# Kernel tuning notes

Hardware: AMD Instinct MI355X
Metric: run time of the kernel (lower is better)

## Reference

```python
import jax, jax.numpy as jnp
import numpy as np

N = 8_000_000  # batch rows; feature dims (1->2->...->2->1) are fixed by P1


def setup_inputs() -> dict:
    key = jax.random.key(0)
    ks = jax.random.split(key, 7)
    return {
        "x": jax.random.normal(ks[0], (N, 1), dtype=jnp.float32),
        "w_in": jax.random.normal(ks[1], (2, 1), dtype=jnp.float32),
        "b_in": jax.random.normal(ks[2], (2,), dtype=jnp.float32),
        "w_hid": jax.random.normal(ks[3], (8, 2, 2), dtype=jnp.float32),
        "b_hid": jax.random.normal(ks[4], (8, 2), dtype=jnp.float32),
        "w_out": jax.random.normal(ks[5], (1, 2), dtype=jnp.float32),
        "b_out": jax.random.normal(ks[6], (1,), dtype=jnp.float32),
    }


def _block(h, W, b):
    # Linear_BasicBlock: y = relu(h @ W.T + b)  (torch nn.Linear convention)
    return jax.nn.relu(jnp.matmul(h, W.T) + b)


def reference(x, w_in, b_in, w_hid, b_hid, w_out, b_out):
    h = _block(x, w_in, b_in)                    # [N,1] -> [N,2]

    def step(h, wb):
        W, b = wb
        return _block(h, W, b), None             # [N,2] -> [N,2]

    h, _ = jax.lax.scan(step, h, (w_hid, b_hid)) # 8 hidden blocks
    out = _block(h, w_out, b_out)                # [N,2] -> [N,1]
    return out
```

## Files before the change

kernel.cpp:

```cpp
#include <hip/hip_runtime.h>

#define NHID 8

__global__ __launch_bounds__(256) void P1_mlp_kernel(
    const float* __restrict__ x,
    const float* __restrict__ w_in, const float* __restrict__ b_in,
    const float* __restrict__ w_hid, const float* __restrict__ b_hid,
    const float* __restrict__ w_out, const float* __restrict__ b_out,
    float* __restrict__ out, int n)
{
    const float wi0 = w_in[0], wi1 = w_in[1];
    const float bi0 = b_in[0], bi1 = b_in[1];
    float wh[NHID][4];
    float bh[NHID][2];
#pragma unroll
    for (int l = 0; l < NHID; ++l) {
        wh[l][0] = w_hid[l * 4 + 0];
        wh[l][1] = w_hid[l * 4 + 1];
        wh[l][2] = w_hid[l * 4 + 2];
        wh[l][3] = w_hid[l * 4 + 3];
        bh[l][0] = b_hid[l * 2 + 0];
        bh[l][1] = b_hid[l * 2 + 1];
    }
    const float wo0 = w_out[0], wo1 = w_out[1], bo = b_out[0];

    const int tid = blockIdx.x * blockDim.x + threadIdx.x;
    const int stride = gridDim.x * blockDim.x;
    const int nv = n >> 2;

    const float4* __restrict__ x4 = (const float4*)x;
    float4* __restrict__ o4 = (float4*)out;

    for (int i = tid; i < nv; i += stride) {
        const float4 xv = x4[i];
        float xin[4] = {xv.x, xv.y, xv.z, xv.w};
        float r[4];
#pragma unroll
        for (int e = 0; e < 4; ++e) {
            float h0 = fmaxf(fmaf(xin[e], wi0, bi0), 0.0f);
            float h1 = fmaxf(fmaf(xin[e], wi1, bi1), 0.0f);
#pragma unroll
            for (int l = 0; l < NHID; ++l) {
                float n0 = fmaxf(fmaf(h1, wh[l][1], fmaf(h0, wh[l][0], bh[l][0])), 0.0f);
                float n1 = fmaxf(fmaf(h1, wh[l][3], fmaf(h0, wh[l][2], bh[l][1])), 0.0f);
                h0 = n0;
                h1 = n1;
            }
            r[e] = fmaxf(fmaf(h1, wo1, fmaf(h0, wo0, bo)), 0.0f);
        }
        float4 ov;
        ov.x = r[0]; ov.y = r[1]; ov.z = r[2]; ov.w = r[3];
        o4[i] = ov;
    }

    const int tail_base = nv << 2;
    const int tail_n = n - tail_base;
    if (tid < tail_n) {
        const float xx = x[tail_base + tid];
        float h0 = fmaxf(fmaf(xx, wi0, bi0), 0.0f);
        float h1 = fmaxf(fmaf(xx, wi1, bi1), 0.0f);
#pragma unroll
        for (int l = 0; l < NHID; ++l) {
            float n0 = fmaxf(fmaf(h1, wh[l][1], fmaf(h0, wh[l][0], bh[l][0])), 0.0f);
            float n1 = fmaxf(fmaf(h1, wh[l][3], fmaf(h0, wh[l][2], bh[l][1])), 0.0f);
            h0 = n0;
            h1 = n1;
        }
        out[tail_base + tid] = fmaxf(fmaf(h1, wo1, fmaf(h0, wo0, bo)), 0.0f);
    }
}

extern "C" void kernel_launch(void* const* d_in, const int* in_sizes, int n_in,
                              void* d_out, int out_size, void* d_ws, size_t ws_size,
                              hipStream_t stream) {
    const float* x     = (const float*)d_in[0];
    const float* w_in  = (const float*)d_in[1];
    const float* b_in  = (const float*)d_in[2];
    const float* w_hid = (const float*)d_in[3];
    const float* b_hid = (const float*)d_in[4];
    const float* w_out = (const float*)d_in[5];
    const float* b_out = (const float*)d_in[6];
    float* out = (float*)d_out;

    const int n = in_sizes[0];
    const int nv = (n + 3) / 4;
    const int block = 256;
    int grid = (nv + block - 1) / block;
    if (grid > 2048) grid = 2048;

    P1_mlp_kernel<<<grid, block, 0, stream>>>(x, w_in, b_in, w_hid, b_hid,
                                              w_out, b_out, out, n);
}
```

Measured before the change: 18.66 us.

## Use packed f32x2 FMA math, nontemporal chunked loads, and full-size grid

Rewrites the per-element MLP so both neurons of each layer are computed with two-wide vector FMA and max, which can map to packed FP32 instructions on CDNA. Replaces the grid-stride loop with a one-shot grid in which each thread handles four consecutive float4 vectors, issuing all loads before any compute. Loads and stores use nontemporal builtins to avoid polluting the cache. This trades more blocks and higher register use for more memory-level parallelism and fewer ALU instructions.

```diff
diff --git a/kernel.cpp b/kernel.cpp
--- a/kernel.cpp
+++ b/kernel.cpp
@@ -1,6 +1,33 @@
 #include <hip/hip_runtime.h>
 
 #define NHID 8
+
+typedef float f32x2 __attribute__((ext_vector_type(2)));
+typedef float f32x4 __attribute__((ext_vector_type(4)));
+
+struct Weights {
+    f32x2 win, bin;
+    f32x2 c0[NHID], c1[NHID], bh[NHID];
+    float wo0, wo1, bo;
+};
+
+__device__ __forceinline__ float mlp_one(float xx, const Weights& W) {
+    const f32x2 zero = {0.0f, 0.0f};
+    f32x2 xb = {xx, xx};
+    f32x2 h = __builtin_elementwise_fma(xb, W.win, W.bin);
+    h = __builtin_elementwise_max(h, zero);
+#pragma unroll
+    for (int l = 0; l < NHID; ++l) {
+        f32x2 h0b = {h.x, h.x};
+        f32x2 h1b = {h.y, h.y};
+        f32x2 t = __builtin_elementwise_fma(h0b, W.c0[l], W.bh[l]);
+        t = __builtin_elementwise_fma(h1b, W.c1[l], t);
+        h = __builtin_elementwise_max(t, zero);
+    }
+    return fmaxf(fmaf(h.y, W.wo1, fmaf(h.x, W.wo0, W.bo)), 0.0f);
+}
+
+#define CHUNK 4
 
 __global__ __launch_bounds__(256) void P1_mlp_kernel(
     const float* __restrict__ x,
@@ -9,64 +36,59 @@
     const float* __restrict__ w_out, const float* __restrict__ b_out,
     float* __restrict__ out, int n)
 {
-    const float wi0 = w_in[0], wi1 = w_in[1];
-    const float bi0 = b_in[0], bi1 = b_in[1];
-    float wh[NHID][4];
-    float bh[NHID][2];
+    Weights W;
+    W.win = (f32x2){w_in[0], w_in[1]};
+    W.bin = (f32x2){b_in[0], b_in[1]};
 #pragma unroll
     for (int l = 0; l < NHID; ++l) {
-        wh[l][0] = w_hid[l * 4 + 0];
-        wh[l][1] = w_hid[l * 4 + 1];
-        wh[l][2] = w_hid[l * 4 + 2];
-        wh[l][3] = w_hid[l * 4 + 3];
-        bh[l][0] = b_hid[l * 2 + 0];
-        bh[l][1] = b_hid[l * 2 + 1];
+        W.c0[l] = (f32x2){w_hid[l * 4 + 0], w_hid[l * 4 + 2]};
+        W.c1[l] = (f32x2){w_hid[l * 4 + 1], w_hid[l * 4 + 3]};
+        W.bh[l] = (f32x2){b_hid[l * 2 + 0], b_hid[l * 2 + 1]};
     }
-    const float wo0 = w_out[0], wo1 = w_out[1], bo = b_out[0];
+    W.wo0 = w_out[0]; W.wo1 = w_out[1]; W.bo = b_out[0];
 
+    const int nv = n >> 2;
     const int tid = blockIdx.x * blockDim.x + threadIdx.x;
-    const int stride = gridDim.x * blockDim.x;
-    const int nv = n >> 2;
+    const int base = tid * CHUNK;
 
-    const float4* __restrict__ x4 = (const float4*)x;
-    float4* __restrict__ o4 = (float4*)out;
+    const f32x4* __restrict__ x4 = (const f32x4*)x;
+    f32x4* __restrict__ o4 = (f32x4*)out;
 
-    for (int i = tid; i < nv; i += stride) {
-        const float4 xv = x4[i];
-        float xin[4] = {xv.x, xv.y, xv.z, xv.w};
-        float r[4];
+    if (base + CHUNK <= nv) {
+        f32x4 v[CHUNK];
 #pragma unroll
-        for (int e = 0; e < 4; ++e) {
-            float h0 = fmaxf(fmaf(xin[e], wi0, bi0), 0.0f);
-            float h1 = fmaxf(fmaf(xin[e], wi1, bi1), 0.0f);
+        for (int j = 0; j < CHUNK; ++j)
+            v[j] = __builtin_nontemporal_load(&x4[base + j]);
+        f32x4 r[CHUNK];
 #pragma unroll
-            for (int l = 0; l < NHID; ++l) {
-                float n0 = fmaxf(fmaf(h1, wh[l][1], fmaf(h0, wh[l][0], bh[l][0])), 0.0f);
-                float n1 = fmaxf(fmaf(h1, wh[l][3], fmaf(h0, wh[l][2], bh[l][1])), 0.0f);
-                h0 = n0;
-                h1 = n1;
+        for (int j = 0; j < CHUNK; ++j) {
+            r[j].x = mlp_one(v[j].x, W);
+            r[j].y = mlp_one(v[j].y, W);
+            r[j].z = mlp_one(v[j].z, W);
+            r[j].w = mlp_one(v[j].w, W);
+        }
+#pragma unroll
+        for (int j = 0; j < CHUNK; ++j)
+            __builtin_nontemporal_store(r[j], &o4[base + j]);
+    } else {
+        for (int j = 0; j < CHUNK; ++j) {
+            int i = base + j;
+            if (i < nv) {
+                f32x4 v = x4[i];
+                f32x4 r;
+                r.x = mlp_one(v.x, W);
+                r.y = mlp_one(v.y, W);
+                r.z = mlp_one(v.z, W);
+                r.w = mlp_one(v.w, W);
+                o4[i] = r;
             }
-            r[e] = fmaxf(fmaf(h1, wo1, fmaf(h0, wo0, bo)), 0.0f);
         }
-        float4 ov;
-        ov.x = r[0]; ov.y = r[1]; ov.z = r[2]; ov.w = r[3];
-        o4[i] = ov;
     }
 
     const int tail_base = nv << 2;
     const int tail_n = n - tail_base;
     if (tid < tail_n) {
-        const float xx = x[tail_base + tid];
-        float h0 = fmaxf(fmaf(xx, wi0, bi0), 0.0f);
-        float h1 = fmaxf(fmaf(xx, wi1, bi1), 0.0f);
-#pragma unroll
-        for (int l = 0; l < NHID; ++l) {
-            float n0 = fmaxf(fmaf(h1, wh[l][1], fmaf(h0, wh[l][0], bh[l][0])), 0.0f);
-            float n1 = fmaxf(fmaf(h1, wh[l][3], fmaf(h0, wh[l][2], bh[l][1])), 0.0f);
-            h0 = n0;
-            h1 = n1;
-        }
-        out[tail_base + tid] = fmaxf(fmaf(h1, wo1, fmaf(h0, wo0, bo)), 0.0f);
+        out[tail_base + tid] = mlp_one(x[tail_base + tid], W);
     }
 }
 
@@ -84,9 +106,9 @@
 
     const int n = in_sizes[0];
     const int nv = (n + 3) / 4;
+    const int threads_needed = (nv + CHUNK - 1) / CHUNK;
     const int block = 256;
-    int grid = (nv + block - 1) / block;
-    if (grid > 2048) grid = 2048;
+    const int grid = (threads_needed + block - 1) / block;
 
     P1_mlp_kernel<<<grid, block, 0, stream>>>(x, w_in, b_in, w_hid, b_hid,
                                               w_out, b_out, out, n);
```

New measurement: 27.86 us. 49.3% more time.
